# Kernel optimization log

Hardware: AMD Instinct MI355X
Metric: run time of the kernel (lower is better)

## Reference

```python
import jax, jax.numpy as jnp
import numpy as np


def setup_inputs() -> dict:
    key = jax.random.key(0)
    ks = jax.random.split(key, 6)
    C, C8, W, H, B = 512, 64, 64, 64, 4
    x = jax.random.normal(ks[0], (B, C, W, H), dtype=jnp.float32)
    Wf = jax.random.normal(ks[1], (C8, C), dtype=jnp.float32) * (1.0 / np.sqrt(C))
    Wg = jax.random.normal(ks[2], (C8, C), dtype=jnp.float32) * (1.0 / np.sqrt(C))
    Wh = jax.random.normal(ks[3], (C8, C), dtype=jnp.float32) * (1.0 / np.sqrt(C))
    Wv = jax.random.normal(ks[4], (C, C8), dtype=jnp.float32) * (1.0 / np.sqrt(C8))
    gamma = jax.random.normal(ks[5], (1,), dtype=jnp.float32)
    return {"x": x, "Wf": Wf, "Wg": Wg, "Wh": Wh, "Wv": Wv, "gamma": gamma}


def reference(x, Wf, Wg, Wh, Wv, gamma):
    b, c, w, h = x.shape
    n = w * h
    xf = x.reshape(b, c, n)                       # [b, c, n]
    # 1x1 convs == channel-mixing GEMMs
    f = jnp.einsum('oc,bcn->bon', Wf, xf)         # [b, c8, n]
    g = jnp.einsum('oc,bcn->bon', Wg, xf)         # [b, c8, n]
    hmap = jnp.einsum('oc,bcn->bon', Wh, xf)      # [b, c8, n]
    # attn_map[b, i, j] = sum_c f[b, c, i] * g[b, c, j]  (f permuted as in torch)
    attn = jnp.einsum('bci,bcj->bij', f, g)       # [b, n, n]
    # unconventional softmax over dim=1 (rows / the i axis)
    attn = jax.nn.softmax(attn, axis=1)
    sa = jnp.einsum('bcn,bnj->bcj', hmap, attn)   # [b, c8, n]
    sa = sa.reshape(b, -1, w, h)                  # [b, c8, w, h]
    sa = jnp.einsum('oc,bcwh->bowh', Wv, sa)      # [b, c, w, h]
    out = sa * gamma[0] + x
    return out, sa
```

## Files before the change

kernel.cpp:

```cpp
#include <hip/hip_runtime.h>
#include <cstddef>

#define BB 4
#define CC 512
#define NN 4096

using half8  = __attribute__((ext_vector_type(8))) _Float16;
using fp16x2 = __attribute__((ext_vector_type(2))) __fp16;
using short8 = __attribute__((ext_vector_type(8))) short;
using us8    = __attribute__((ext_vector_type(8))) unsigned short;
using f32x4  = __attribute__((ext_vector_type(4))) float;
using f32x16 = __attribute__((ext_vector_type(16))) float;

__device__ __forceinline__ unsigned short f2bf(float x) {
    unsigned int u = __float_as_uint(x);
    u += 0x7fffu + ((u >> 16) & 1u);
    return (unsigned short)(u >> 16);
}

__global__ __launch_bounds__(256) void prep_kernel(
    const float* __restrict__ Wf, const float* __restrict__ Wg,
    const float* __restrict__ Wh, const float* __restrict__ Wv,
    _Float16* __restrict__ Wc16, _Float16* __restrict__ Wv16)
{
    int idx = blockIdx.x * 256 + threadIdx.x;
    int stride = gridDim.x * 256;
    const int N1 = 192 * 512, N2 = 512 * 64;
    for (int i = idx; i < N1 + N2; i += stride) {
        if (i < N1) {
            int row = i >> 9, c = i & 511;
            const float* src = (row < 64) ? Wf : ((row < 128) ? Wg : Wh);
            float sc = (row >= 64 && row < 128) ? 1.4426950408889634f : 1.0f;
            Wc16[i] = (_Float16)(sc * src[(row & 63) * 512 + c]);
        } else {
            int k = i - N1;
            Wv16[k] = (_Float16)Wv[k];
        }
    }
}

__global__ __launch_bounds__(256) void proj_kernel(
    const float* __restrict__ x, const _Float16* __restrict__ Wc16,
    _Float16* __restrict__ Kf, _Float16* __restrict__ Qf,
    unsigned short* __restrict__ Vt)
{
    __shared__ float xsT[2][32][68];
    const int t    = threadIdx.x;
    const int w    = t >> 6;
    const int lane = t & 63;
    const int lh   = lane & 15;
    const int qd   = lane >> 4;
    const int b    = blockIdx.x >> 7;
    const int i0   = (blockIdx.x & 127) << 5;

    f32x4 acc[3][2];
    #pragma unroll
    for (int ot = 0; ot < 3; ot++)
        #pragma unroll
        for (int it = 0; it < 2; it++) { acc[ot][it][0]=0.f; acc[ot][it][1]=0.f; acc[ot][it][2]=0.f; acc[ot][it][3]=0.f; }

    const int ti8 = t & 7;
    const int tc2 = t >> 3;
    const float* xbase = x + (size_t)b*CC*NN + i0 + ti8*4;
    const _Float16* wbase = Wc16 + (size_t)(w*48 + lh)*512 + qd*8;

    float4 st0, st1;
    half8  wcur[2][3], wnxt[2][3];

#define LOADX(ck) do {                                                        \
    st0 = *(const float4*)(xbase + (size_t)((ck)*64 + tc2)*NN);               \
    st1 = *(const float4*)(xbase + (size_t)((ck)*64 + 32 + tc2)*NN);          \
} while (0)
#define STOREX(p_) do {                                                       \
    xsT[p_][ti8*4+0][tc2]    = st0.x; xsT[p_][ti8*4+1][tc2]    = st0.y;       \
    xsT[p_][ti8*4+2][tc2]    = st0.z; xsT[p_][ti8*4+3][tc2]    = st0.w;       \
    xsT[p_][ti8*4+0][32+tc2] = st1.x; xsT[p_][ti8*4+1][32+tc2] = st1.y;       \
    xsT[p_][ti8*4+2][32+tc2] = st1.z; xsT[p_][ti8*4+3][32+tc2] = st1.w;       \
} while (0)
#define LOADW(ck, WD) do {                                                    \
    _Pragma("unroll")                                                         \
    for (int ks_ = 0; ks_ < 2; ks_++)                                         \
        _Pragma("unroll")                                                     \
        for (int ot_ = 0; ot_ < 3; ot_++)                                     \
            WD[ks_][ot_] = *(const half8*)(wbase + (size_t)(ot_*16)*512 + (ck)*64 + ks_*32); \
} while (0)

    LOADX(0); STOREX(0);
    LOADW(0, wcur);
    __syncthreads();

    #pragma unroll
    for (int ck = 0; ck < 8; ck++) {
        const int p = ck & 1;
        if (ck < 7) { LOADX(ck + 1); LOADW(ck + 1, wnxt); }

        #pragma unroll
        for (int ks = 0; ks < 2; ks++) {
            half8 xf[2];
            #pragma unroll
            for (int it = 0; it < 2; it++) {
                const float* xr = &xsT[p][it*16 + lh][ks*32 + qd*8];
                f32x4 xa = *(const f32x4*)xr;
                f32x4 xb = *(const f32x4*)(xr + 4);
                union { fp16x2 h2[4]; half8 h8; } u;
                u.h2[0] = __builtin_amdgcn_cvt_pkrtz(xa[0], xa[1]);
                u.h2[1] = __builtin_amdgcn_cvt_pkrtz(xa[2], xa[3]);
                u.h2[2] = __builtin_amdgcn_cvt_pkrtz(xb[0], xb[1]);
                u.h2[3] = __builtin_amdgcn_cvt_pkrtz(xb[2], xb[3]);
                xf[it] = u.h8;
            }
            #pragma unroll
            for (int ot = 0; ot < 3; ot++)
                #pragma unroll
                for (int it = 0; it < 2; it++)
                    acc[ot][it] = __builtin_amdgcn_mfma_f32_16x16x32_f16(wcur[ks][ot], xf[it], acc[ot][it], 0, 0, 0);
        }

        if (ck < 7) {
            STOREX(p ^ 1);
            #pragma unroll
            for (int ks_ = 0; ks_ < 2; ks_++)
                #pragma unroll
                for (int ot_ = 0; ot_ < 3; ot_++)
                    wcur[ks_][ot_] = wnxt[ks_][ot_];
        }
        __syncthreads();
    }
#undef LOADX
#undef STOREX
#undef LOADW

    #pragma unroll
    for (int ot = 0; ot < 3; ot++) {
        int g16 = w*3 + ot;
        int m   = g16 >> 2;
        int obase = (g16 & 3)*16 + qd*4;
        #pragma unroll
        for (int it = 0; it < 2; it++) {
            int ig = i0 + it*16 + lh;
            #pragma unroll
            for (int r = 0; r < 4; r++) {
                float v = acc[ot][it][r];
                int ol = obase + r;
                if (m == 0)       Kf[((size_t)b*NN + ig)*64 + ol] = (_Float16)v;
                else if (m == 1)  Qf[((size_t)b*NN + ig)*64 + ol] = (_Float16)v;
                else              Vt[((size_t)b*64 + ol)*NN + ig] = f2bf(v);
            }
        }
    }
}

template<int SPLITS>
__global__ __launch_bounds__(256, 3) void attn_kernel(
    const _Float16* __restrict__ Kf, const _Float16* __restrict__ Qf,
    const unsigned short* __restrict__ Vt,
    _Float16* __restrict__ Po16, float* __restrict__ Pl)
{
    static_assert(NN % SPLITS == 0, "split");
    constexpr int KS  = NN / SPLITS;
    constexpr int NCH = KS / 64;

    __shared__ __align__(16) unsigned short Kb2[2][64*64];
    __shared__ __align__(16) unsigned short Vb2[2][64*64];

    const int t    = threadIdx.x;
    const int wv   = t >> 6;
    const int lane = t & 63;
    const int il   = lane & 31;
    const int h    = lane >> 5;

    const int p  = blockIdx.x;
    const int v  = (p & 7) * (SPLITS * 16) + (p >> 3);
    const int jt = v & 31;
    const int bs = v >> 5;
    const int b  = bs / SPLITS;
    const int s  = bs % SPLITS;
    const int j0w  = jt*128 + wv*32;
    const int koff = s * KS;

    half8 qfr[4];
    {
        const _Float16* qp = Qf + ((size_t)b*NN + j0w + il)*64 + h*8;
        #pragma unroll
        for (int sl = 0; sl < 4; sl++) qfr[sl] = *(const half8*)(qp + sl*16);
    }

    f32x16 o_acc[2];
    #pragma unroll
    for (int dt = 0; dt < 2; dt++)
        #pragma unroll
        for (int r = 0; r < 16; r++) o_acc[dt][r] = 0.f;
    float l4[4] = {0.f, 0.f, 0.f, 0.f};

    const int fx = (il & 7) ^ ((il >> 3) & 3);

    const int ik0 = t >> 3;
    const int fk0 = (ik0 & 7) ^ ((ik0 >> 3) & 3);
    const int sw  = ((t & 7) ^ fk0) << 3;
    const int ik1 = ik0 + 32;
    const _Float16*       gk0 = Kf + ((size_t)b*NN + koff + ik0)*64 + sw;
    const _Float16*       gk1 = Kf + ((size_t)b*NN + koff + ik1)*64 + sw;
    const unsigned short* gv0 = Vt + ((size_t)b*64 + ik0)*NN + koff + sw;
    const unsigned short* gv1 = Vt + ((size_t)b*64 + ik1)*NN + koff + sw;

#define STAGE(ck, pb) do {                                                          \
    const size_t o64_ = (size_t)(ck)*64;                                            \
    __builtin_amdgcn_global_load_lds(                                               \
        (const __attribute__((address_space(1))) void*)(gk0 + o64_*64),             \
        (__attribute__((address_space(3))) void*)&Kb2[pb][(wv*64)*8], 16, 0, 0);    \
    __builtin_amdgcn_global_load_lds(                                               \
        (const __attribute__((address_space(1))) void*)(gk1 + o64_*64),             \
        (__attribute__((address_space(3))) void*)&Kb2[pb][(256 + wv*64)*8], 16, 0, 0); \
    __builtin_amdgcn_global_load_lds(                                               \
        (const __attribute__((address_space(1))) void*)(gv0 + o64_),                \
        (__attribute__((address_space(3))) void*)&Vb2[pb][(wv*64)*8], 16, 0, 0);    \
    __builtin_amdgcn_global_load_lds(                                               \
        (const __attribute__((address_space(1))) void*)(gv1 + o64_),                \
        (__attribute__((address_space(3))) void*)&Vb2[pb][(256 + wv*64)*8], 16, 0, 0); \
    } while (0)

    STAGE(0, 0);
    __syncthreads();

    for (int ck = 0; ck < NCH; ck++) {
        const int cb = ck & 1;
        if (ck + 1 < NCH) STAGE(ck + 1, cb ^ 1);

        const unsigned short* Kb = Kb2[cb];
        const unsigned short* Vb = Vb2[cb];

        #pragma unroll
        for (int isub = 0; isub < 2; isub++) {
            const int irow = isub*32 + il;
            const unsigned short* kr = Kb + irow*64;
            f32x16 sc;
            #pragma unroll
            for (int r = 0; r < 16; r++) sc[r] = 0.f;
            #pragma unroll
            for (int sl = 0; sl < 4; sl++) {
                half8 kf = *(const half8*)(kr + (((sl*2 + h) ^ fx) << 3));
                sc = __builtin_amdgcn_mfma_f32_32x32x16_f16(kf, qfr[sl], sc, 0, 0, 0);
            }

            float pq[16];
            #pragma unroll
            for (int r = 0; r < 16; r++) pq[r] = exp2f(sc[r]);
            #pragma unroll
            for (int r = 0; r < 16; r++) l4[r & 3] += pq[r];

            unsigned wA[8];
            #pragma unroll
            for (int k = 0; k < 8; k++)
                asm("v_cvt_pk_bf16_f32 %0, %1, %2" : "=v"(wA[k]) : "v"(pq[2*k]), "v"(pq[2*k+1]));
            asm("v_permlane32_swap_b32 %0, %1" : "+v"(wA[0]), "+v"(wA[2]));
            asm("v_permlane32_swap_b32 %0, %1" : "+v"(wA[1]), "+v"(wA[3]));
            asm("v_permlane32_swap_b32 %0, %1" : "+v"(wA[4]), "+v"(wA[6]));
            asm("v_permlane32_swap_b32 %0, %1" : "+v"(wA[5]), "+v"(wA[7]));

            union { unsigned u[4]; short8 s8; } pa0, pa1;
            pa0.u[0]=wA[0]; pa0.u[1]=wA[1]; pa0.u[2]=wA[2]; pa0.u[3]=wA[3];
            pa1.u[0]=wA[4]; pa1.u[1]=wA[5]; pa1.u[2]=wA[6]; pa1.u[3]=wA[7];

            #pragma unroll
            for (int isl = 0; isl < 2; isl++) {
                const short8 paf = isl ? pa1.s8 : pa0.s8;
                const int vc = isub*4 + isl*2 + h;
                #pragma unroll
                for (int dt = 0; dt < 2; dt++) {
                    const int drow = dt*32 + il;
                    short8 vf = *(const short8*)(Vb + drow*64 + ((vc ^ fx) << 3));
                    o_acc[dt] = __builtin_amdgcn_mfma_f32_32x32x16_bf16(paf, vf, o_acc[dt], 0, 0, 0);
                }
            }
        }
        __syncthreads();
    }
#undef STAGE

    float l_acc  = (l4[0] + l4[1]) + (l4[2] + l4[3]);
    float l_full = l_acc + __shfl_xor(l_acc, 32);
    float inv = 1.0f / l_full;

    const size_t pbase = (size_t)(s*4 + b)*NN + j0w;
    #pragma unroll
    for (int r = 0; r < 16; r++) {
        const int jr = (r & 3) + 8*(r >> 2) + 4*h;
        const float invr = __shfl(inv, jr);
        #pragma unroll
        for (int dt = 0; dt < 2; dt++)
            Po16[(pbase + jr)*64 + dt*32 + il] = (_Float16)(o_acc[dt][r] * invr);
    }
    if (h == 0) Pl[pbase + il] = l_full;
}

template<int SPLITS>
__global__ __launch_bounds__(256) void outproj_kernel(
    const _Float16* __restrict__ Po16, const float* __restrict__ Pl,
    const _Float16* __restrict__ Wv16,
    const float* __restrict__ x, const float* __restrict__ gamma,
    float* __restrict__ out1, float* __restrict__ out2)
{
    __shared__ __align__(16) _Float16 sbM[16][72];
    __shared__ float Osh[4][16][20];
    const int t    = threadIdx.x;
    const int w    = t >> 6;
    const int lane = t & 63;
    const int lh   = lane & 15;
    const int qd   = lane >> 4;
    const int b    = blockIdx.x >> 8;
    const int j0   = (blockIdx.x & 255) << 4;
    const float g  = gamma[0];

    if (t < 128) {
        const int jj = t & 15, d8 = t >> 4;
        float os[8];
        #pragma unroll
        for (int k = 0; k < 8; k++) os[k] = 0.f;
        float lsum = 0.f;
        #pragma unroll
        for (int s = 0; s < SPLITS; s++) {
            const size_t base = (size_t)(s*4 + b)*NN + j0 + jj;
            half8 vv = *(const half8*)(Po16 + base*64 + d8*8);
            float l  = Pl[base];
            #pragma unroll
            for (int k = 0; k < 8; k++) os[k] = fmaf(l, (float)vv[k], os[k]);
            lsum += l;
        }
        const float inv = 1.0f / lsum;
        union { fp16x2 h2[4]; half8 h8; } u;
        #pragma unroll
        for (int k = 0; k < 4; k++)
            u.h2[k] = __builtin_amdgcn_cvt_pkrtz(os[2*k]*inv, os[2*k+1]*inv);
        *(half8*)&sbM[jj][d8*8] = u.h8;
    }
    __syncthreads();

    const half8 sb0 = *(const half8*)&sbM[lh][qd*8];
    const half8 sb1 = *(const half8*)&sbM[lh][32 + qd*8];

    const int o_loc = lane >> 2;
    const int j4    = (lane & 3) * 4;

    #pragma unroll 2
    for (int ot8 = 0; ot8 < 8; ot8++) {
        const int ot = w*8 + ot8;

        const size_t idx = ((size_t)b*CC + ot*16 + o_loc)*NN + j0 + j4;
        const f32x4 xv = *(const f32x4*)(x + idx);

        const size_t wbase = (size_t)(ot*16 + lh)*64 + qd*8;
        half8 a0 = *(const half8*)(Wv16 + wbase);
        half8 a1 = *(const half8*)(Wv16 + wbase + 32);

        f32x4 acc;
        acc[0]=0.f; acc[1]=0.f; acc[2]=0.f; acc[3]=0.f;
        acc = __builtin_amdgcn_mfma_f32_16x16x32_f16(a0, sb0, acc, 0, 0, 0);
        acc = __builtin_amdgcn_mfma_f32_16x16x32_f16(a1, sb1, acc, 0, 0, 0);

        #pragma unroll
        for (int r = 0; r < 4; r++)
            Osh[w][qd*4 + r][lh] = acc[r];
        asm volatile("s_waitcnt lgkmcnt(0)" ::: "memory");

        f32x4 vv = *(const f32x4*)&Osh[w][o_loc][j4];
        *(f32x4*)(out2 + idx) = vv;
        f32x4 r1;
        r1[0] = fmaf(g, vv[0], xv[0]); r1[1] = fmaf(g, vv[1], xv[1]);
        r1[2] = fmaf(g, vv[2], xv[2]); r1[3] = fmaf(g, vv[3], xv[3]);
        *(f32x4*)(out1 + idx) = r1;
        asm volatile("s_waitcnt lgkmcnt(0)" ::: "memory");
    }
}

extern "C" void kernel_launch(void* const* d_in, const int* in_sizes, int n_in,
                              void* d_out, int out_size, void* d_ws, size_t ws_size,
                              hipStream_t stream) {
    const float* x     = (const float*)d_in[0];
    const float* Wf    = (const float*)d_in[1];
    const float* Wg    = (const float*)d_in[2];
    const float* Wh    = (const float*)d_in[3];
    const float* Wv    = (const float*)d_in[4];
    const float* gamma = (const float*)d_in[5];

    float* out1 = (float*)d_out;
    float* out2 = out1 + (size_t)BB*CC*NN;

    const size_t BND = (size_t)BB*NN*64;
    const size_t need8 = BND*2*3 + BND*2*8 + (size_t)8*BB*NN*4
                       + (size_t)192*512*2 + (size_t)512*64*2;
    const int SPL = (ws_size >= need8) ? 8 : 4;

    char* wp = (char*)d_ws;
    _Float16*       Kf   = (_Float16*)wp;        wp += BND*2;
    _Float16*       Qf   = (_Float16*)wp;        wp += BND*2;
    unsigned short* Vt   = (unsigned short*)wp;  wp += BND*2;
    _Float16*       Po16 = (_Float16*)wp;        wp += BND*2*SPL;
    float*          Pl   = (float*)wp;           wp += (size_t)SPL*BB*NN*4;
    _Float16*       Wc16 = (_Float16*)wp;        wp += (size_t)192*512*2;
    _Float16*       Wv16 = (_Float16*)wp;

    prep_kernel<<<dim3(64), dim3(256), 0, stream>>>(Wf, Wg, Wh, Wv, Wc16, Wv16);
    proj_kernel<<<dim3(BB*128), dim3(256), 0, stream>>>(x, Wc16, Kf, Qf, Vt);
    if (SPL == 8) {
        attn_kernel<8><<<dim3(128*8), dim3(256), 0, stream>>>(Kf, Qf, Vt, Po16, Pl);
        outproj_kernel<8><<<dim3(BB*256), dim3(256), 0, stream>>>(Po16, Pl, Wv16, x, gamma, out1, out2);
    } else {
        attn_kernel<4><<<dim3(128*4), dim3(256), 0, stream>>>(Kf, Qf, Vt, Po16, Pl);
        outproj_kernel<4><<<dim3(BB*256), dim3(256), 0, stream>>>(Po16, Pl, Wv16, x, gamma, out1, out2);
    }
}
```

Before: 164.6 us.

## Load K/V fragments directly from global memory instead of LDS double buffering

Removes the shared-memory double-buffered staging of K and V tiles and their block-wide barriers. Each wave now reads its MFMA operand fragments straight from global memory into registers, 32 keys per iteration, and the occupancy hint rises from 3 to 4 blocks per CU. Dropping LDS and barriers frees occupancy and removes the synchronization cost. The four waves in a block now each fetch the same K/V data separately, so the kernel depends on L1/L2 hits and on global-load latency being hidden by more resident waves.

```diff
diff --git a/kernel.cpp b/kernel.cpp
--- a/kernel.cpp
+++ b/kernel.cpp
@@ -151,17 +151,14 @@
 }
 
 template<int SPLITS>
-__global__ __launch_bounds__(256, 3) void attn_kernel(
+__global__ __launch_bounds__(256, 4) void attn_kernel(
     const _Float16* __restrict__ Kf, const _Float16* __restrict__ Qf,
     const unsigned short* __restrict__ Vt,
     _Float16* __restrict__ Po16, float* __restrict__ Pl)
 {
     static_assert(NN % SPLITS == 0, "split");
-    constexpr int KS  = NN / SPLITS;
-    constexpr int NCH = KS / 64;
-
-    __shared__ __align__(16) unsigned short Kb2[2][64*64];
-    __shared__ __align__(16) unsigned short Vb2[2][64*64];
+    constexpr int KS = NN / SPLITS;
+    constexpr int NT = KS / 32;
 
     const int t    = threadIdx.x;
     const int wv   = t >> 6;
@@ -192,90 +189,56 @@
         for (int r = 0; r < 16; r++) o_acc[dt][r] = 0.f;
     float l4[4] = {0.f, 0.f, 0.f, 0.f};
 
-    const int fx = (il & 7) ^ ((il >> 3) & 3);
-
-    const int ik0 = t >> 3;
-    const int fk0 = (ik0 & 7) ^ ((ik0 >> 3) & 3);
-    const int sw  = ((t & 7) ^ fk0) << 3;
-    const int ik1 = ik0 + 32;
-    const _Float16*       gk0 = Kf + ((size_t)b*NN + koff + ik0)*64 + sw;
-    const _Float16*       gk1 = Kf + ((size_t)b*NN + koff + ik1)*64 + sw;
-    const unsigned short* gv0 = Vt + ((size_t)b*64 + ik0)*NN + koff + sw;
-    const unsigned short* gv1 = Vt + ((size_t)b*64 + ik1)*NN + koff + sw;
-
-#define STAGE(ck, pb) do {                                                          \
-    const size_t o64_ = (size_t)(ck)*64;                                            \
-    __builtin_amdgcn_global_load_lds(                                               \
-        (const __attribute__((address_space(1))) void*)(gk0 + o64_*64),             \
-        (__attribute__((address_space(3))) void*)&Kb2[pb][(wv*64)*8], 16, 0, 0);    \
-    __builtin_amdgcn_global_load_lds(                                               \
-        (const __attribute__((address_space(1))) void*)(gk1 + o64_*64),             \
-        (__attribute__((address_space(3))) void*)&Kb2[pb][(256 + wv*64)*8], 16, 0, 0); \
-    __builtin_amdgcn_global_load_lds(                                               \
-        (const __attribute__((address_space(1))) void*)(gv0 + o64_),                \
-        (__attribute__((address_space(3))) void*)&Vb2[pb][(wv*64)*8], 16, 0, 0);    \
-    __builtin_amdgcn_global_load_lds(                                               \
-        (const __attribute__((address_space(1))) void*)(gv1 + o64_),                \
-        (__attribute__((address_space(3))) void*)&Vb2[pb][(256 + wv*64)*8], 16, 0, 0); \
-    } while (0)
-
-    STAGE(0, 0);
-    __syncthreads();
-
-    for (int ck = 0; ck < NCH; ck++) {
-        const int cb = ck & 1;
-        if (ck + 1 < NCH) STAGE(ck + 1, cb ^ 1);
-
-        const unsigned short* Kb = Kb2[cb];
-        const unsigned short* Vb = Vb2[cb];
-
-        #pragma unroll
-        for (int isub = 0; isub < 2; isub++) {
-            const int irow = isub*32 + il;
-            const unsigned short* kr = Kb + irow*64;
-            f32x16 sc;
-            #pragma unroll
-            for (int r = 0; r < 16; r++) sc[r] = 0.f;
-            #pragma unroll
-            for (int sl = 0; sl < 4; sl++) {
-                half8 kf = *(const half8*)(kr + (((sl*2 + h) ^ fx) << 3));
-                sc = __builtin_amdgcn_mfma_f32_32x32x16_f16(kf, qfr[sl], sc, 0, 0, 0);
-            }
-
-            float pq[16];
-            #pragma unroll
-            for (int r = 0; r < 16; r++) pq[r] = exp2f(sc[r]);
-            #pragma unroll
-            for (int r = 0; r < 16; r++) l4[r & 3] += pq[r];
-
-            unsigned wA[8];
-            #pragma unroll
-            for (int k = 0; k < 8; k++)
-                asm("v_cvt_pk_bf16_f32 %0, %1, %2" : "=v"(wA[k]) : "v"(pq[2*k]), "v"(pq[2*k+1]));
-            asm("v_permlane32_swap_b32 %0, %1" : "+v"(wA[0]), "+v"(wA[2]));
-            asm("v_permlane32_swap_b32 %0, %1" : "+v"(wA[1]), "+v"(wA[3]));
-            asm("v_permlane32_swap_b32 %0, %1" : "+v"(wA[4]), "+v"(wA[6]));
-            asm("v_permlane32_swap_b32 %0, %1" : "+v"(wA[5]), "+v"(wA[7]));
-
-            union { unsigned u[4]; short8 s8; } pa0, pa1;
-            pa0.u[0]=wA[0]; pa0.u[1]=wA[1]; pa0.u[2]=wA[2]; pa0.u[3]=wA[3];
-            pa1.u[0]=wA[4]; pa1.u[1]=wA[5]; pa1.u[2]=wA[6]; pa1.u[3]=wA[7];
-
-            #pragma unroll
-            for (int isl = 0; isl < 2; isl++) {
-                const short8 paf = isl ? pa1.s8 : pa0.s8;
-                const int vc = isub*4 + isl*2 + h;
-                #pragma unroll
-                for (int dt = 0; dt < 2; dt++) {
-                    const int drow = dt*32 + il;
-                    short8 vf = *(const short8*)(Vb + drow*64 + ((vc ^ fx) << 3));
-                    o_acc[dt] = __builtin_amdgcn_mfma_f32_32x32x16_bf16(paf, vf, o_acc[dt], 0, 0, 0);
-                }
-            }
-        }
-        __syncthreads();
-    }
-#undef STAGE
+    const _Float16*       Kb  = Kf + ((size_t)b*NN + koff + il)*64 + h*8;
+    const unsigned short* Vb0 = Vt + ((size_t)(b*64      + il))*NN + koff + h*8;
+    const unsigned short* Vb1 = Vt + ((size_t)(b*64 + 32 + il))*NN + koff + h*8;
+
+    #pragma unroll 2
+    for (int nt = 0; nt < NT; ++nt) {
+        const _Float16* kp = Kb + (size_t)(nt*32)*64;
+        const int ib = nt*32;
+
+        half8  kf0 = *(const half8*)(kp);
+        half8  kf1 = *(const half8*)(kp + 16);
+        half8  kf2 = *(const half8*)(kp + 32);
+        half8  kf3 = *(const half8*)(kp + 48);
+        short8 v00 = *(const short8*)(Vb0 + ib);
+        short8 v01 = *(const short8*)(Vb1 + ib);
+        short8 v10 = *(const short8*)(Vb0 + ib + 16);
+        short8 v11 = *(const short8*)(Vb1 + ib + 16);
+
+        f32x16 sc;
+        #pragma unroll
+        for (int r = 0; r < 16; r++) sc[r] = 0.f;
+        sc = __builtin_amdgcn_mfma_f32_32x32x16_f16(kf0, qfr[0], sc, 0, 0, 0);
+        sc = __builtin_amdgcn_mfma_f32_32x32x16_f16(kf1, qfr[1], sc, 0, 0, 0);
+        sc = __builtin_amdgcn_mfma_f32_32x32x16_f16(kf2, qfr[2], sc, 0, 0, 0);
+        sc = __builtin_amdgcn_mfma_f32_32x32x16_f16(kf3, qfr[3], sc, 0, 0, 0);
+
+        float pq[16];
+        #pragma unroll
+        for (int r = 0; r < 16; r++) pq[r] = exp2f(sc[r]);
+        #pragma unroll
+        for (int r = 0; r < 16; r++) l4[r & 3] += pq[r];
+
+        unsigned wA[8];
+        #pragma unroll
+        for (int k = 0; k < 8; k++)
+            asm("v_cvt_pk_bf16_f32 %0, %1, %2" : "=v"(wA[k]) : "v"(pq[2*k]), "v"(pq[2*k+1]));
+        asm("v_permlane32_swap_b32 %0, %1" : "+v"(wA[0]), "+v"(wA[2]));
+        asm("v_permlane32_swap_b32 %0, %1" : "+v"(wA[1]), "+v"(wA[3]));
+        asm("v_permlane32_swap_b32 %0, %1" : "+v"(wA[4]), "+v"(wA[6]));
+        asm("v_permlane32_swap_b32 %0, %1" : "+v"(wA[5]), "+v"(wA[7]));
+
+        union { unsigned u[4]; short8 s8; } pa0, pa1;
+        pa0.u[0]=wA[0]; pa0.u[1]=wA[1]; pa0.u[2]=wA[2]; pa0.u[3]=wA[3];
+        pa1.u[0]=wA[4]; pa1.u[1]=wA[5]; pa1.u[2]=wA[6]; pa1.u[3]=wA[7];
+
+        o_acc[0] = __builtin_amdgcn_mfma_f32_32x32x16_bf16(pa0.s8, v00, o_acc[0], 0, 0, 0);
+        o_acc[1] = __builtin_amdgcn_mfma_f32_32x32x16_bf16(pa0.s8, v01, o_acc[1], 0, 0, 0);
+        o_acc[0] = __builtin_amdgcn_mfma_f32_32x32x16_bf16(pa1.s8, v10, o_acc[0], 0, 0, 0);
+        o_acc[1] = __builtin_amdgcn_mfma_f32_32x32x16_bf16(pa1.s8, v11, o_acc[1], 0, 0, 0);
+    }
 
     float l_acc  = (l4[0] + l4[1]) + (l4[2] + l4[3]);
     float l_full = l_acc + __shfl_xor(l_acc, 32);
```

After: 203.7 us. +23.7%, slower.
